# Performance work log

Measured on AMD Instinct MI355X. Metric: run time of the kernel, lower is better.

The kernel has to match this reference:

```python
import jax, jax.numpy as jnp
import numpy as np

B, C, HEADS, W, Hh = 8, 512, 8, 32, 32
D = C // HEADS  # 64 per-head dim
N = W * Hh      # 1024 spatial tokens


def setup_inputs() -> dict:
    key = jax.random.key(0)
    ks = jax.random.split(key, 10)
    s = 1.0 / np.sqrt(C)
    return {
        "x": jax.random.normal(ks[0], (B, C, W, Hh), dtype=jnp.float32),
        "Wq": jax.random.normal(ks[1], (C, C), dtype=jnp.float32) * s,
        "bq": jax.random.normal(ks[2], (C,), dtype=jnp.float32) * 0.01,
        "Wk": jax.random.normal(ks[3], (C, C), dtype=jnp.float32) * s,
        "bk": jax.random.normal(ks[4], (C,), dtype=jnp.float32) * 0.01,
        "Wv": jax.random.normal(ks[5], (C, C), dtype=jnp.float32) * s,
        "bv": jax.random.normal(ks[6], (C,), dtype=jnp.float32) * 0.01,
        "rel_h": jax.random.normal(ks[7], (1, HEADS, D, 1, Hh), dtype=jnp.float32),
        "rel_w": jax.random.normal(ks[8], (1, HEADS, D, W, 1), dtype=jnp.float32),
    }


def reference(x, Wq, bq, Wk, bk, Wv, bv, rel_h, rel_w):
    b = x.shape[0]
    xf = x.reshape(b, C, N)  # [B, C, N] — 1x1 conv == per-position linear
    proj = lambda Wm, bm: (jnp.einsum('oc,bcn->bon', Wm, xf) + bm[None, :, None]).reshape(b, HEADS, D, N)
    q = proj(Wq, bq)  # [B, H, D, N]
    k = proj(Wk, bk)
    v = proj(Wv, bv)
    # content-content: q^T k -> [B, H, N, N]
    cc = jnp.einsum('bhdn,bhdm->bhnm', q, k)
    # relative position bias: (rel_h + rel_w) -> [H, D, N], then rel^T @ q
    rel = (rel_h + rel_w).reshape(HEADS, D, N)
    cp = jnp.einsum('hdn,bhdm->bhnm', rel, q)  # [B, H, N, N]
    attn = jax.nn.softmax(cc + cp, axis=-1)
    # out = v @ attn^T : out[d,m] = sum_n v[d,n] * attn[m,n]
    out = jnp.einsum('bhdn,bhmn->bhdm', v, attn)  # [B, H, D, N]
    return out.reshape(b, C, W, Hh)
```

## Files before the change

### kernel.cpp

```cpp
#include <hip/hip_runtime.h>

typedef short short8 __attribute__((ext_vector_type(8)));
typedef _Float16 half8 __attribute__((ext_vector_type(8)));
typedef _Float16 half4 __attribute__((ext_vector_type(4)));
typedef float f32x4 __attribute__((ext_vector_type(4)));

__device__ __forceinline__ void glds16(const void* g, void* l) {
    __builtin_amdgcn_global_load_lds(
        (const __attribute__((address_space(1))) unsigned int*)g,
        (__attribute__((address_space(3))) unsigned int*)l, 16, 0, 0);
}


__global__ void k_pack_w(const float* __restrict__ Wq, const float* __restrict__ Wk,
                         const float* __restrict__ Wv, const float* __restrict__ bq,
                         const float* __restrict__ bk, const float* __restrict__ bv,
                         _Float16* __restrict__ Wf, float* __restrict__ bias2) {
    int t = blockIdx.x * 256 + threadIdx.x;
    int m = t >> 6;
    int c8 = (t & 63) << 3;
    const float* src = (m < 512) ? (Wq + m * 512)
                     : (m < 1024 ? (Wk + (m - 512) * 512) : (Wv + (m - 1024) * 512));
    float4 v0 = *(const float4*)(src + c8);
    float4 v1 = *(const float4*)(src + c8 + 4);
    half8 o;
    o[0] = (_Float16)v0.x; o[1] = (_Float16)v0.y; o[2] = (_Float16)v0.z; o[3] = (_Float16)v0.w;
    o[4] = (_Float16)v1.x; o[5] = (_Float16)v1.y; o[6] = (_Float16)v1.z; o[7] = (_Float16)v1.w;
    *(half8*)(Wf + (size_t)m * 512 + c8) = o;
    if (t < 1536)
        bias2[t] = (t < 512) ? bq[t] : (t < 1024 ? bk[t - 512] : bv[t - 1024]);
}

__global__ void k_prep_x(const float* __restrict__ x, _Float16* __restrict__ xTf) {
    __shared__ float xs[64][65];
    int nt = blockIdx.x * 64, ct = blockIdx.y * 64, b = blockIdx.z;
    int t = threadIdx.x;
    const float* xb = x + ((size_t)b * 512 + ct) * 1024 + nt;
#pragma unroll
    for (int p = 0; p < 4; ++p) {
        int c = p * 16 + (t >> 4), n4 = (t & 15) * 4;
        float4 v = *(const float4*)(xb + (size_t)c * 1024 + n4);
        xs[c][n4] = v.x; xs[c][n4 + 1] = v.y; xs[c][n4 + 2] = v.z; xs[c][n4 + 3] = v.w;
    }
    __syncthreads();
    int nl = t >> 2, part = t & 3;
    _Float16* rowp = xTf + ((size_t)b * 1024 + nt + nl) * 512;
#pragma unroll
    for (int g = 0; g < 2; ++g) {
        half8 o;
#pragma unroll
        for (int j = 0; j < 8; ++j)
            o[j] = (_Float16)xs[part * 16 + g * 8 + j][nl];
        *(half8*)(rowp + ct + part * 16 + g * 8) = o;
    }
}

__global__ void k_prep_rel(const float* __restrict__ rel_h, const float* __restrict__ rel_w,
                           _Float16* __restrict__ rel2) {
    int tid = blockIdx.x * 256 + threadIdx.x;
    int h = tid >> 13;
    int rem = tid & 8191;
    int n = rem >> 3;
    int g = rem & 7;
    int hh = n & 31, ww = n >> 5;
    half8 o;
#pragma unroll
    for (int j = 0; j < 8; ++j) {
        int d = g * 8 + j;
        o[j] = (_Float16)(rel_h[(h * 64 + d) * 32 + hh] + rel_w[(h * 64 + d) * 32 + ww]);
    }
    *(half8*)(rel2 + ((size_t)h * 1024 + n) * 64 + g * 8) = o;
}

__global__ __launch_bounds__(256, 3) void k_proj(const _Float16* __restrict__ Wf,
                                                 const _Float16* __restrict__ xTf,
                                                 const float* __restrict__ bias2,
                                                 _Float16* __restrict__ q2,
                                                 _Float16* __restrict__ k2,
                                                 _Float16* __restrict__ vb) {
    __shared__ __align__(16) _Float16 As[8192];
    __shared__ __align__(16) _Float16 Bs[8192];
    int t = threadIdx.x;
    int lane = t & 63, w = t >> 6;
    int lm = lane & 15, lq = lane >> 4;
    int wr = (w >> 1) * 64, wc = (w & 1) * 64;
    int mb = blockIdx.y * 128, nb = blockIdx.x * 128, b = blockIdx.z;
    int rl = lane >> 2;
    int csw = ((lane & 3) ^ ((lane >> 3) & 3)) * 8;
    const _Float16* Ag0 = Wf + (size_t)(mb + w * 32 + rl) * 512 + csw;
    const _Float16* Ag1 = Ag0 + 16 * 512;
    const _Float16* Bg0 = xTf + ((size_t)b * 1024 + nb + w * 32 + rl) * 512 + csw;
    const _Float16* Bg1 = Bg0 + 16 * 512;
    f32x4 acc[4][4];
#pragma unroll
    for (int i = 0; i < 4; ++i)
#pragma unroll
        for (int j = 0; j < 4; ++j) acc[i][j] = {0.f, 0.f, 0.f, 0.f};
    int fsw = (lq ^ ((lm >> 1) & 3)) * 8;
    for (int k0 = 0; k0 < 512; k0 += 64) {
#pragma unroll
        for (int kh = 0; kh < 2; ++kh) {
            int ko = k0 + kh * 32;
            glds16(Ag0 + ko, &As[kh * 4096 + (w * 32) * 32]);
            glds16(Ag1 + ko, &As[kh * 4096 + (w * 32 + 16) * 32]);
            glds16(Bg0 + ko, &Bs[kh * 4096 + (w * 32) * 32]);
            glds16(Bg1 + ko, &Bs[kh * 4096 + (w * 32 + 16) * 32]);
        }
        __syncthreads();
#pragma unroll
        for (int kh = 0; kh < 2; ++kh) {
            half8 af[4], bfr[4];
#pragma unroll
            for (int mt = 0; mt < 4; ++mt)
                af[mt] = *(half8*)&As[kh * 4096 + (wr + mt * 16 + lm) * 32 + fsw];
#pragma unroll
            for (int nt = 0; nt < 4; ++nt)
                bfr[nt] = *(half8*)&Bs[kh * 4096 + (wc + nt * 16 + lm) * 32 + fsw];
#pragma unroll
            for (int mt = 0; mt < 4; ++mt)
#pragma unroll
                for (int nt = 0; nt < 4; ++nt)
                    acc[mt][nt] = __builtin_amdgcn_mfma_f32_16x16x32_f16(af[mt], bfr[nt], acc[mt][nt], 0, 0, 0);
        }
        __syncthreads();
    }
    int sect = mb >> 9;
    int hloc = ((mb & 511) + wr) >> 6;
    size_t bh = (size_t)b * 8 + hloc;
    if (sect < 2) {
        _Float16* dst = (sect == 0 ? q2 : k2) + bh * 1024 * 64;
#pragma unroll
        for (int mt = 0; mt < 4; ++mt) {
            int d0 = mt * 16 + lq * 4;
            float bi0 = bias2[mb + wr + d0];
            float bi1 = bias2[mb + wr + d0 + 1];
            float bi2 = bias2[mb + wr + d0 + 2];
            float bi3 = bias2[mb + wr + d0 + 3];
#pragma unroll
            for (int nt = 0; nt < 4; ++nt) {
                int n = nb + wc + nt * 16 + lm;
                half4 o;
                o[0] = (_Float16)(acc[mt][nt][0] + bi0);
                o[1] = (_Float16)(acc[mt][nt][1] + bi1);
                o[2] = (_Float16)(acc[mt][nt][2] + bi2);
                o[3] = (_Float16)(acc[mt][nt][3] + bi3);
                *(half4*)(dst + (size_t)n * 64 + d0) = o;
            }
        }
    } else {
        _Float16* dst = vb + bh * 64 * 1024;
#pragma unroll
        for (int mt = 0; mt < 4; ++mt)
#pragma unroll
            for (int reg = 0; reg < 4; ++reg) {
                int d = mt * 16 + lq * 4 + reg;
                float bi = bias2[mb + wr + d];
#pragma unroll
                for (int nt = 0; nt < 4; ++nt) {
                    int n = nb + wc + nt * 16 + lm;
                    dst[(size_t)d * 1024 + n] = (_Float16)(acc[mt][nt][reg] + bi);
                }
            }
    }
}

__global__ __launch_bounds__(256, 4) void k_attn(const _Float16* __restrict__ q2,
                                                 const _Float16* __restrict__ k2,
                                                 const _Float16* __restrict__ rel2,
                                                 const _Float16* __restrict__ vb,
                                                 float* __restrict__ out) {
    __shared__ __align__(16) char pool[35840];
    _Float16* kb_s = (_Float16*)pool;
    _Float16* v_s  = (_Float16*)(pool + 17408);
    _Float16* p_s  = (_Float16*)(pool + 26624);
    int t = threadIdx.x;
    int lane = t & 63, w = t >> 6;
    int lm = lane & 15, lq = lane >> 4;
    int lin = blockIdx.x;
    int mt0 = lin >> 6;
    int bh_ = lin & 63;
    int h = bh_ & 7, b = bh_ >> 3;
    size_t bh = (size_t)b * 8 + h;
    const _Float16* q2b = q2 + bh * 1024 * 64;
    const _Float16* k2b = k2 + bh * 1024 * 64;
    const _Float16* relb = rel2 + (size_t)h * 1024 * 64;
    const _Float16* vbb = vb + bh * 64 * 1024;
    float* outb = out + bh * 64 * 1024 + mt0 * 64;

    int r = t >> 2, part = t & 3;
    const _Float16* ksrc = ((part < 2) ? (k2b + part * 32) : (q2b + (part - 2) * 32));
    int vc = (t & 3) * 16;
    const _Float16* vsrcb = vbb + (size_t)r * 1024 + vc;
    _Float16* kdst = kb_s + r * 136 + part * 32;
    _Float16* vdst = v_s + r * 72 + vc;

    uint4 kc0, kc1, kc2, kc3, vv0, vv1;
    {
        const uint4* s_ = (const uint4*)(ksrc + (size_t)r * 64);
        kc0 = s_[0]; kc1 = s_[1]; kc2 = s_[2]; kc3 = s_[3];
        const uint4* v_ = (const uint4*)vsrcb;
        vv0 = v_[0]; vv1 = v_[1];
    }

    {
        int n = mt0 * 64 + r;
        const _Float16* src = (part < 2) ? (q2b + (size_t)n * 64 + part * 32)
                                         : (relb + (size_t)n * 64 + (part - 2) * 32);
        ((uint4*)kdst)[0] = ((const uint4*)src)[0];
        ((uint4*)kdst)[1] = ((const uint4*)src)[1];
        ((uint4*)kdst)[2] = ((const uint4*)src)[2];
        ((uint4*)kdst)[3] = ((const uint4*)src)[3];
    }
    __syncthreads();
    half8 ah[4];
#pragma unroll
    for (int kk = 0; kk < 4; ++kk)
        ah[kk] = *(half8*)&kb_s[(w * 16 + lm) * 136 + kk * 32 + lq * 8];
    f32x4 acco[4];
#pragma unroll
    for (int i = 0; i < 4; ++i) acco[i] = {0.f, 0.f, 0.f, 0.f};
    float mrun = -3e38f, lrun = 0.f;

    for (int kt = 0; kt < 16; ++kt) {
        ((uint4*)kdst)[0] = kc0;
        ((uint4*)kdst)[1] = kc1;
        ((uint4*)kdst)[2] = kc2;
        ((uint4*)kdst)[3] = kc3;
        ((uint4*)vdst)[0] = vv0;
        ((uint4*)vdst)[1] = vv1;
        __syncthreads();
        int nn = ((kt + 1) & 15) * 64;
        const uint4* s_ = (const uint4*)(ksrc + (size_t)(nn + r) * 64);
        uint4 kn0 = s_[0], kn1 = s_[1], kn2 = s_[2], kn3 = s_[3];
        const uint4* v_ = (const uint4*)(vsrcb + nn);
        uint4 vn0 = v_[0], vn1 = v_[1];
        f32x4 sac[4];
#pragma unroll
        for (int ct = 0; ct < 4; ++ct) sac[ct] = {0.f, 0.f, 0.f, 0.f};
#pragma unroll
        for (int ct = 0; ct < 4; ++ct) {
            half8 kf[4];
#pragma unroll
            for (int kk = 0; kk < 4; ++kk)
                kf[kk] = *(half8*)&kb_s[(ct * 16 + lm) * 136 + kk * 32 + lq * 8];
#pragma unroll
            for (int kk = 0; kk < 4; ++kk)
                sac[ct] = __builtin_amdgcn_mfma_f32_16x16x32_f16(kf[kk], ah[kk], sac[ct], 0, 0, 0);
        }
        float mx = -3e38f;
#pragma unroll
        for (int ct = 0; ct < 4; ++ct)
#pragma unroll
            for (int reg = 0; reg < 4; ++reg) mx = fmaxf(mx, sac[ct][reg]);
        mx = fmaxf(mx, __shfl_xor(mx, 16));
        mx = fmaxf(mx, __shfl_xor(mx, 32));
        float mnew = fmaxf(mrun, mx);
        float al_ = __expf(mrun - mnew);
        float ps[4][4];
        float rs = 0.f;
#pragma unroll
        for (int ct = 0; ct < 4; ++ct)
#pragma unroll
            for (int reg = 0; reg < 4; ++reg) {
                float p = __expf(sac[ct][reg] - mnew);
                ps[ct][reg] = p;
                rs += p;
            }
        rs += __shfl_xor(rs, 16);
        rs += __shfl_xor(rs, 32);
        lrun = lrun * al_ + rs;
        mrun = mnew;
#pragma unroll
        for (int dt = 0; dt < 4; ++dt) {
            acco[dt][0] *= al_; acco[dt][1] *= al_;
            acco[dt][2] *= al_; acco[dt][3] *= al_;
        }
#pragma unroll
        for (int ct = 0; ct < 4; ++ct) {
            half4 o;
            o[0] = (_Float16)ps[ct][0]; o[1] = (_Float16)ps[ct][1];
            o[2] = (_Float16)ps[ct][2]; o[3] = (_Float16)ps[ct][3];
            *(half4*)&p_s[(w * 16 + lm) * 72 + ct * 16 + lq * 4] = o;
        }
        half8 pfr[2];
#pragma unroll
        for (int ch = 0; ch < 2; ++ch)
            pfr[ch] = *(half8*)&p_s[(w * 16 + lm) * 72 + ch * 32 + lq * 8];
#pragma unroll
        for (int dt = 0; dt < 4; ++dt) {
            half8 vf0 = *(half8*)&v_s[(dt * 16 + lm) * 72 + lq * 8];
            half8 vf1 = *(half8*)&v_s[(dt * 16 + lm) * 72 + 32 + lq * 8];
            acco[dt] = __builtin_amdgcn_mfma_f32_16x16x32_f16(vf0, pfr[0], acco[dt], 0, 0, 0);
            acco[dt] = __builtin_amdgcn_mfma_f32_16x16x32_f16(vf1, pfr[1], acco[dt], 0, 0, 0);
        }
        __syncthreads();
        kc0 = kn0; kc1 = kn1; kc2 = kn2; kc3 = kn3;
        vv0 = vn0; vv1 = vn1;
    }
    float li = 1.f / lrun;
#pragma unroll
    for (int dt = 0; dt < 4; ++dt)
#pragma unroll
        for (int reg = 0; reg < 4; ++reg) {
            int d = dt * 16 + lq * 4 + reg;
            outb[(size_t)d * 1024 + w * 16 + lm] = acco[dt][reg] * li;
        }
}

extern "C" void kernel_launch(void* const* d_in, const int* in_sizes, int n_in,
                              void* d_out, int out_size, void* d_ws, size_t ws_size,
                              hipStream_t stream) {
    const float* x     = (const float*)d_in[0];
    const float* Wq    = (const float*)d_in[1];
    const float* bq    = (const float*)d_in[2];
    const float* Wk    = (const float*)d_in[3];
    const float* bk    = (const float*)d_in[4];
    const float* Wv    = (const float*)d_in[5];
    const float* bv    = (const float*)d_in[6];
    const float* rel_h = (const float*)d_in[7];
    const float* rel_w = (const float*)d_in[8];
    char* ws = (char*)d_ws;
    _Float16* Wf   = (_Float16*)(ws);
    float* bias2   = (float*)(ws + 1572864);
    _Float16* xTf  = (_Float16*)(ws + 1579008);
    _Float16* q2   = (_Float16*)(ws + 9967616);
    _Float16* k2   = (_Float16*)(ws + 18356224);
    _Float16* vb   = (_Float16*)(ws + 26744832);
    _Float16* rel2 = (_Float16*)(ws + 35133440);
    float* out = (float*)d_out;

    hipLaunchKernelGGL(k_pack_w,   dim3(384),      dim3(256), 0, stream, Wq, Wk, Wv, bq, bk, bv, Wf, bias2);
    hipLaunchKernelGGL(k_prep_x,   dim3(16, 8, 8), dim3(256), 0, stream, x, xTf);
    hipLaunchKernelGGL(k_prep_rel, dim3(256),      dim3(256), 0, stream, rel_h, rel_w, rel2);
    hipLaunchKernelGGL(k_proj,     dim3(8, 12, 8), dim3(256), 0, stream, Wf, xTf, bias2, q2, k2, vb);
    hipLaunchKernelGGL(k_attn,     dim3(1024),     dim3(256), 0, stream, q2, k2, rel2, vb, out);
}
```

Baseline: 161.2 us.

## Merge prep kernels, fold log2e into q, and XOR-swizzle attention LDS tiles

```diff
diff --git a/kernel.cpp b/kernel.cpp
--- a/kernel.cpp
+++ b/kernel.cpp
@@ -1,6 +1,5 @@
 #include <hip/hip_runtime.h>
 
-typedef short short8 __attribute__((ext_vector_type(8)));
 typedef _Float16 half8 __attribute__((ext_vector_type(8)));
 typedef _Float16 half4 __attribute__((ext_vector_type(4)));
 typedef float f32x4 __attribute__((ext_vector_type(4)));
@@ -12,64 +11,66 @@
 }
 
 
-__global__ void k_pack_w(const float* __restrict__ Wq, const float* __restrict__ Wk,
-                         const float* __restrict__ Wv, const float* __restrict__ bq,
-                         const float* __restrict__ bk, const float* __restrict__ bv,
-                         _Float16* __restrict__ Wf, float* __restrict__ bias2) {
-    int t = blockIdx.x * 256 + threadIdx.x;
-    int m = t >> 6;
-    int c8 = (t & 63) << 3;
-    const float* src = (m < 512) ? (Wq + m * 512)
-                     : (m < 1024 ? (Wk + (m - 512) * 512) : (Wv + (m - 1024) * 512));
-    float4 v0 = *(const float4*)(src + c8);
-    float4 v1 = *(const float4*)(src + c8 + 4);
-    half8 o;
-    o[0] = (_Float16)v0.x; o[1] = (_Float16)v0.y; o[2] = (_Float16)v0.z; o[3] = (_Float16)v0.w;
-    o[4] = (_Float16)v1.x; o[5] = (_Float16)v1.y; o[6] = (_Float16)v1.z; o[7] = (_Float16)v1.w;
-    *(half8*)(Wf + (size_t)m * 512 + c8) = o;
-    if (t < 1536)
-        bias2[t] = (t < 512) ? bq[t] : (t < 1024 ? bk[t - 512] : bv[t - 1024]);
-}
-
-__global__ void k_prep_x(const float* __restrict__ x, _Float16* __restrict__ xTf) {
+__global__ void k_prep_all(const float* __restrict__ Wq, const float* __restrict__ Wk,
+                           const float* __restrict__ Wv, const float* __restrict__ bq,
+                           const float* __restrict__ bk, const float* __restrict__ bv,
+                           const float* __restrict__ x, const float* __restrict__ rel_h,
+                           const float* __restrict__ rel_w, _Float16* __restrict__ Wf,
+                           float* __restrict__ bias2, _Float16* __restrict__ xTf,
+                           _Float16* __restrict__ rel2) {
     __shared__ float xs[64][65];
-    int nt = blockIdx.x * 64, ct = blockIdx.y * 64, b = blockIdx.z;
-    int t = threadIdx.x;
-    const float* xb = x + ((size_t)b * 512 + ct) * 1024 + nt;
-#pragma unroll
-    for (int p = 0; p < 4; ++p) {
-        int c = p * 16 + (t >> 4), n4 = (t & 15) * 4;
-        float4 v = *(const float4*)(xb + (size_t)c * 1024 + n4);
-        xs[c][n4] = v.x; xs[c][n4 + 1] = v.y; xs[c][n4 + 2] = v.z; xs[c][n4 + 3] = v.w;
-    }
-    __syncthreads();
-    int nl = t >> 2, part = t & 3;
-    _Float16* rowp = xTf + ((size_t)b * 1024 + nt + nl) * 512;
-#pragma unroll
-    for (int g = 0; g < 2; ++g) {
+    int bid = blockIdx.x;
+    if (bid < 384) {
+        int t = bid * 256 + threadIdx.x;
+        int m = t >> 6;
+        int c8 = (t & 63) << 3;
+        const float* src = (m < 512) ? (Wq + m * 512)
+                         : (m < 1024 ? (Wk + (m - 512) * 512) : (Wv + (m - 1024) * 512));
+        float4 v0 = *(const float4*)(src + c8);
+        float4 v1 = *(const float4*)(src + c8 + 4);
         half8 o;
-#pragma unroll
-        for (int j = 0; j < 8; ++j)
-            o[j] = (_Float16)xs[part * 16 + g * 8 + j][nl];
-        *(half8*)(rowp + ct + part * 16 + g * 8) = o;
-    }
-}
-
-__global__ void k_prep_rel(const float* __restrict__ rel_h, const float* __restrict__ rel_w,
-                           _Float16* __restrict__ rel2) {
-    int tid = blockIdx.x * 256 + threadIdx.x;
-    int h = tid >> 13;
-    int rem = tid & 8191;
-    int n = rem >> 3;
-    int g = rem & 7;
-    int hh = n & 31, ww = n >> 5;
-    half8 o;
-#pragma unroll
-    for (int j = 0; j < 8; ++j) {
-        int d = g * 8 + j;
-        o[j] = (_Float16)(rel_h[(h * 64 + d) * 32 + hh] + rel_w[(h * 64 + d) * 32 + ww]);
-    }
-    *(half8*)(rel2 + ((size_t)h * 1024 + n) * 64 + g * 8) = o;
+        o[0] = (_Float16)v0.x; o[1] = (_Float16)v0.y; o[2] = (_Float16)v0.z; o[3] = (_Float16)v0.w;
+        o[4] = (_Float16)v1.x; o[5] = (_Float16)v1.y; o[6] = (_Float16)v1.z; o[7] = (_Float16)v1.w;
+        *(half8*)(Wf + (size_t)m * 512 + c8) = o;
+        if (t < 1536)
+            bias2[t] = (t < 512) ? bq[t] : (t < 1024 ? bk[t - 512] : bv[t - 1024]);
+    } else if (bid < 1408) {
+        int i = bid - 384;
+        int nt = (i & 15) << 6, ct = ((i >> 4) & 7) << 6, b = i >> 7;
+        int t = threadIdx.x;
+        const float* xb = x + ((size_t)b * 512 + ct) * 1024 + nt;
+#pragma unroll
+        for (int p = 0; p < 4; ++p) {
+            int c = p * 16 + (t >> 4), n4 = (t & 15) * 4;
+            float4 v = *(const float4*)(xb + (size_t)c * 1024 + n4);
+            xs[c][n4] = v.x; xs[c][n4 + 1] = v.y; xs[c][n4 + 2] = v.z; xs[c][n4 + 3] = v.w;
+        }
+        __syncthreads();
+        int nl = t >> 2, part = t & 3;
+        _Float16* rowp = xTf + ((size_t)b * 1024 + nt + nl) * 512;
+#pragma unroll
+        for (int g = 0; g < 2; ++g) {
+            half8 o;
+#pragma unroll
+            for (int j = 0; j < 8; ++j)
+                o[j] = (_Float16)xs[part * 16 + g * 8 + j][nl];
+            *(half8*)(rowp + ct + part * 16 + g * 8) = o;
+        }
+    } else {
+        int tid = (bid - 1408) * 256 + threadIdx.x;
+        int h = tid >> 13;
+        int rem = tid & 8191;
+        int n = rem >> 3;
+        int g = rem & 7;
+        int hh = n & 31, ww = n >> 5;
+        half8 o;
+#pragma unroll
+        for (int j = 0; j < 8; ++j) {
+            int d = g * 8 + j;
+            o[j] = (_Float16)(rel_h[(h * 64 + d) * 32 + hh] + rel_w[(h * 64 + d) * 32 + ww]);
+        }
+        *(half8*)(rel2 + ((size_t)h * 1024 + n) * 64 + g * 8) = o;
+    }
 }
 
 __global__ __launch_bounds__(256, 3) void k_proj(const _Float16* __restrict__ Wf,
@@ -128,6 +129,7 @@
     int hloc = ((mb & 511) + wr) >> 6;
     size_t bh = (size_t)b * 8 + hloc;
     if (sect < 2) {
+        float sc = (sect == 0) ? 1.44269504089f : 1.0f;
         _Float16* dst = (sect == 0 ? q2 : k2) + bh * 1024 * 64;
 #pragma unroll
         for (int mt = 0; mt < 4; ++mt) {
@@ -140,10 +142,10 @@
             for (int nt = 0; nt < 4; ++nt) {
                 int n = nb + wc + nt * 16 + lm;
                 half4 o;
-                o[0] = (_Float16)(acc[mt][nt][0] + bi0);
-                o[1] = (_Float16)(acc[mt][nt][1] + bi1);
-                o[2] = (_Float16)(acc[mt][nt][2] + bi2);
-                o[3] = (_Float16)(acc[mt][nt][3] + bi3);
+                o[0] = (_Float16)((acc[mt][nt][0] + bi0) * sc);
+                o[1] = (_Float16)((acc[mt][nt][1] + bi1) * sc);
+                o[2] = (_Float16)((acc[mt][nt][2] + bi2) * sc);
+                o[3] = (_Float16)((acc[mt][nt][3] + bi3) * sc);
                 *(half4*)(dst + (size_t)n * 64 + d0) = o;
             }
         }
@@ -169,10 +171,9 @@
                                                  const _Float16* __restrict__ rel2,
                                                  const _Float16* __restrict__ vb,
                                                  float* __restrict__ out) {
-    __shared__ __align__(16) char pool[35840];
-    _Float16* kb_s = (_Float16*)pool;
-    _Float16* v_s  = (_Float16*)(pool + 17408);
-    _Float16* p_s  = (_Float16*)(pool + 26624);
+    __shared__ __align__(16) _Float16 kb4[4][64][32];
+    __shared__ __align__(16) _Float16 v2[2][64][32];
+    __shared__ __align__(16) _Float16 p2[2][64][32];
     int t = threadIdx.x;
     int lane = t & 63, w = t >> 6;
     int lm = lane & 15, lq = lane >> 4;
@@ -188,11 +189,13 @@
     float* outb = out + bh * 64 * 1024 + mt0 * 64;
 
     int r = t >> 2, part = t & 3;
+    int ssw = ((r >> 1) & 3) * 8;
     const _Float16* ksrc = ((part < 2) ? (k2b + part * 32) : (q2b + (part - 2) * 32));
-    int vc = (t & 3) * 16;
-    const _Float16* vsrcb = vbb + (size_t)r * 1024 + vc;
-    _Float16* kdst = kb_s + r * 136 + part * 32;
-    _Float16* vdst = v_s + r * 72 + vc;
+    _Float16* kbase = &kb4[part][r][0];
+    int cv = (t & 3) >> 1, uv = ((t & 3) & 1) * 2;
+    const _Float16* vsrcb = vbb + (size_t)r * 1024 + (t & 3) * 16;
+    _Float16* vbase = &v2[cv][r][0];
+    int slm = ((lm >> 1) & 3) * 8;
 
     uint4 kc0, kc1, kc2, kc3, vv0, vv1;
     {
@@ -206,28 +209,28 @@
         int n = mt0 * 64 + r;
         const _Float16* src = (part < 2) ? (q2b + (size_t)n * 64 + part * 32)
                                          : (relb + (size_t)n * 64 + (part - 2) * 32);
-        ((uint4*)kdst)[0] = ((const uint4*)src)[0];
-        ((uint4*)kdst)[1] = ((const uint4*)src)[1];
-        ((uint4*)kdst)[2] = ((const uint4*)src)[2];
-        ((uint4*)kdst)[3] = ((const uint4*)src)[3];
+        *(uint4*)(kbase + (0 ^ ssw))  = ((const uint4*)src)[0];
+        *(uint4*)(kbase + (8 ^ ssw))  = ((const uint4*)src)[1];
+        *(uint4*)(kbase + (16 ^ ssw)) = ((const uint4*)src)[2];
+        *(uint4*)(kbase + (24 ^ ssw)) = ((const uint4*)src)[3];
     }
     __syncthreads();
     half8 ah[4];
 #pragma unroll
     for (int kk = 0; kk < 4; ++kk)
-        ah[kk] = *(half8*)&kb_s[(w * 16 + lm) * 136 + kk * 32 + lq * 8];
+        ah[kk] = *(half8*)&kb4[kk][w * 16 + lm][(lq * 8) ^ slm];
     f32x4 acco[4];
 #pragma unroll
     for (int i = 0; i < 4; ++i) acco[i] = {0.f, 0.f, 0.f, 0.f};
     float mrun = -3e38f, lrun = 0.f;
 
     for (int kt = 0; kt < 16; ++kt) {
-        ((uint4*)kdst)[0] = kc0;
-        ((uint4*)kdst)[1] = kc1;
-        ((uint4*)kdst)[2] = kc2;
-        ((uint4*)kdst)[3] = kc3;
-        ((uint4*)vdst)[0] = vv0;
-        ((uint4*)vdst)[1] = vv1;
+        *(uint4*)(kbase + (0 ^ ssw))  = kc0;
+        *(uint4*)(kbase + (8 ^ ssw))  = kc1;
+        *(uint4*)(kbase + (16 ^ ssw)) = kc2;
+        *(uint4*)(kbase + (24 ^ ssw)) = kc3;
+        *(uint4*)(vbase + ((uv * 8) ^ ssw))       = vv0;
+        *(uint4*)(vbase + (((uv + 1) * 8) ^ ssw)) = vv1;
         __syncthreads();
         int nn = ((kt + 1) & 15) * 64;
         const uint4* s_ = (const uint4*)(ksrc + (size_t)(nn + r) * 64);
@@ -242,7 +245,7 @@
             half8 kf[4];
 #pragma unroll
             for (int kk = 0; kk < 4; ++kk)
-                kf[kk] = *(half8*)&kb_s[(ct * 16 + lm) * 136 + kk * 32 + lq * 8];
+                kf[kk] = *(half8*)&kb4[kk][ct * 16 + lm][(lq * 8) ^ slm];
 #pragma unroll
             for (int kk = 0; kk < 4; ++kk)
                 sac[ct] = __builtin_amdgcn_mfma_f32_16x16x32_f16(kf[kk], ah[kk], sac[ct], 0, 0, 0);
@@ -255,17 +258,20 @@
         mx = fmaxf(mx, __shfl_xor(mx, 16));
         mx = fmaxf(mx, __shfl_xor(mx, 32));
         float mnew = fmaxf(mrun, mx);
-        float al_ = __expf(mrun - mnew);
-        float ps[4][4];
+        float al_ = exp2f(mrun - mnew);
         float rs = 0.f;
 #pragma unroll
-        for (int ct = 0; ct < 4; ++ct)
-#pragma unroll
-            for (int reg = 0; reg < 4; ++reg) {
-                float p = __expf(sac[ct][reg] - mnew);
-                ps[ct][reg] = p;
-                rs += p;
-            }
+        for (int ct = 0; ct < 4; ++ct) {
+            float p0 = exp2f(sac[ct][0] - mnew);
+            float p1 = exp2f(sac[ct][1] - mnew);
+            float p2v = exp2f(sac[ct][2] - mnew);
+            float p3 = exp2f(sac[ct][3] - mnew);
+            rs += (p0 + p1) + (p2v + p3);
+            int up = ct * 2 + (lq >> 1);
+            int cp = up >> 2, ui = up & 3, hh = lq & 1;
+            half4 o; o[0] = (_Float16)p0; o[1] = (_Float16)p1; o[2] = (_Float16)p2v; o[3] = (_Float16)p3;
+            *(half4*)&p2[cp][w * 16 + lm][((ui * 8) ^ slm) + hh * 4] = o;
+        }
         rs += __shfl_xor(rs, 16);
         rs += __shfl_xor(rs, 32);
         lrun = lrun * al_ + rs;
@@ -275,21 +281,14 @@
             acco[dt][0] *= al_; acco[dt][1] *= al_;
             acco[dt][2] *= al_; acco[dt][3] *= al_;
         }
-#pragma unroll
-        for (int ct = 0; ct < 4; ++ct) {
-            half4 o;
-            o[0] = (_Float16)ps[ct][0]; o[1] = (_Float16)ps[ct][1];
-            o[2] = (_Float16)ps[ct][2]; o[3] = (_Float16)ps[ct][3];
-            *(half4*)&p_s[(w * 16 + lm) * 72 + ct * 16 + lq * 4] = o;
-        }
         half8 pfr[2];
 #pragma unroll
         for (int ch = 0; ch < 2; ++ch)
-            pfr[ch] = *(half8*)&p_s[(w * 16 + lm) * 72 + ch * 32 + lq * 8];
+            pfr[ch] = *(half8*)&p2[ch][w * 16 + lm][(lq * 8) ^ slm];
 #pragma unroll
         for (int dt = 0; dt < 4; ++dt) {
-            half8 vf0 = *(half8*)&v_s[(dt * 16 + lm) * 72 + lq * 8];
-            half8 vf1 = *(half8*)&v_s[(dt * 16 + lm) * 72 + 32 + lq * 8];
+            half8 vf0 = *(half8*)&v2[0][dt * 16 + lm][(lq * 8) ^ slm];
+            half8 vf1 = *(half8*)&v2[1][dt * 16 + lm][(lq * 8) ^ slm];
             acco[dt] = __builtin_amdgcn_mfma_f32_16x16x32_f16(vf0, pfr[0], acco[dt], 0, 0, 0);
             acco[dt] = __builtin_amdgcn_mfma_f32_16x16x32_f16(vf1, pfr[1], acco[dt], 0, 0, 0);
         }
@@ -329,9 +328,8 @@
     _Float16* rel2 = (_Float16*)(ws + 35133440);
     float* out = (float*)d_out;
 
-    hipLaunchKernelGGL(k_pack_w,   dim3(384),      dim3(256), 0, stream, Wq, Wk, Wv, bq, bk, bv, Wf, bias2);
-    hipLaunchKernelGGL(k_prep_x,   dim3(16, 8, 8), dim3(256), 0, stream, x, xTf);
-    hipLaunchKernelGGL(k_prep_rel, dim3(256),      dim3(256), 0, stream, rel_h, rel_w, rel2);
+    hipLaunchKernelGGL(k_prep_all, dim3(1664),     dim3(256), 0, stream,
+                       Wq, Wk, Wv, bq, bk, bv, x, rel_h, rel_w, Wf, bias2, xTf, rel2);
     hipLaunchKernelGGL(k_proj,     dim3(8, 12, 8), dim3(256), 0, stream, Wf, xTf, bias2, q2, k2, vb);
     hipLaunchKernelGGL(k_attn,     dim3(1024),     dim3(256), 0, stream, q2, k2, rel2, vb, out);
 }
```

After: 163.1 us. About the same (+1.2%).
